# Kernel optimization log

Hardware: AMD Instinct MI355X
Metric: run time of the kernel (lower is better)

## Reference

```python
import jax, jax.numpy as jnp
import numpy as np

B, S, D, H = 2, 2048, 1024, 16
HD = D // H  # head_dim = 64


def setup_inputs() -> dict:
    key = jax.random.key(0)
    ks = jax.random.split(key, 12)
    w_scale = 1.0 / np.sqrt(D)
    return {
        "x": jax.random.normal(ks[0], (B, S, D), dtype=jnp.float32),
        "cause_mask": jax.random.randint(ks[1], (B, S), 0, 2) > 0,
        "effect_mask": jax.random.randint(ks[2], (B, S), 0, 2) > 0,
        "intervention_strength": jnp.float32(1.0),
        "Wq": jax.random.normal(ks[3], (D, D), dtype=jnp.float32) * w_scale,
        "bq": jnp.zeros((D,), dtype=jnp.float32),
        "Wk": jax.random.normal(ks[4], (D, D), dtype=jnp.float32) * w_scale,
        "bk": jnp.zeros((D,), dtype=jnp.float32),
        "Wv": jax.random.normal(ks[5], (D, D), dtype=jnp.float32) * w_scale,
        "bv": jnp.zeros((D,), dtype=jnp.float32),
        "Wo": jax.random.normal(ks[6], (D, D), dtype=jnp.float32) * w_scale,
        "bo": jnp.zeros((D,), dtype=jnp.float32),
    }


def reference(x, cause_mask, effect_mask, intervention_strength,
              Wq, bq, Wk, bk, Wv, bv, Wo, bo):
    b, s, d = x.shape
    # QKV projections -> [b, H, s, HD]
    q = (x @ Wq + bq).reshape(b, s, H, HD).transpose(0, 2, 1, 3)
    k = (x @ Wk + bk).reshape(b, s, H, HD).transpose(0, 2, 1, 3)
    v = (x @ Wv + bv).reshape(b, s, H, HD).transpose(0, 2, 1, 3)

    scores = jnp.einsum("bhqd,bhkd->bhqk", q, k) / jnp.sqrt(jnp.float32(HD))

    # Intervention mask: cause tokens on the query axis, effect on the key axis.
    # Faithful to source: both 'effect_to_cause' and 'cause_to_effect' are the
    # same boolean product, so multiplier = 1 - s*m + 0.5*s*m.
    cm = cause_mask[:, None, :, None]  # [b,1,s,1] query axis
    em = effect_mask[:, None, None, :]  # [b,1,1,s] key axis
    m = (cm & em).astype(scores.dtype)  # [b,1,s,s], broadcasts over heads
    imask = 1.0 - intervention_strength * m + 0.5 * intervention_strength * m
    scores = scores * imask

    attn = jax.nn.softmax(scores, axis=-1)  # dropout is identity in eval
    out = jnp.einsum("bhqk,bhkd->bhqd", attn, v)
    out = out.transpose(0, 2, 1, 3).reshape(b, s, d)
    return out @ Wo + bo
```

## Files before the change

kernel.cpp:

```cpp
#include <hip/hip_runtime.h>
#include <hip/hip_bf16.h>


typedef __attribute__((ext_vector_type(8))) short bf16x8;
typedef __attribute__((ext_vector_type(4))) float f32x4;

__device__ __forceinline__ unsigned short f2b(float f) {
  union { float f; unsigned u; } x; x.f = f;
  unsigned r = x.u + 0x7FFFu + ((x.u >> 16) & 1u);
  return (unsigned short)(r >> 16);
}

__device__ __forceinline__ unsigned short f2b_n(float f) {
  __hip_bfloat16 h = __float2bfloat16(f);
  union { __hip_bfloat16 h; unsigned short u; } c; c.h = h;
  return c.u;
}

__device__ __forceinline__ float fexp2(float x) {
#if __has_builtin(__builtin_amdgcn_exp2f)
  return __builtin_amdgcn_exp2f(x);
#else
  return __expf(x * 0.6931471805599453f);
#endif
}

__device__ __forceinline__ void gl_lds16(const unsigned short* g, unsigned short* l) {
  __builtin_amdgcn_global_load_lds(
      (const __attribute__((address_space(1))) unsigned int*)g,
      (__attribute__((address_space(3))) unsigned int*)l, 16, 0, 0);
}


__global__ __launch_bounds__(256) void cvt_x_kernel(const float* __restrict__ x,
                                                    unsigned short* __restrict__ xb, int n4) {
  int i = blockIdx.x * 256 + threadIdx.x;
  if (i >= n4) return;
  float4 v = ((const float4*)x)[i];
  ushort4 o;
  o.x = f2b(v.x); o.y = f2b(v.y); o.z = f2b(v.z); o.w = f2b(v.w);
  ((ushort4*)xb)[i] = o;
}

__global__ __launch_bounds__(256) void cvt_w4_kernel(
    const float* __restrict__ W0, const float* __restrict__ W1,
    const float* __restrict__ W2, const float* __restrict__ W3,
    unsigned short* __restrict__ WtBase) {
  __shared__ float t[64][33];
  const int z = blockIdx.z;
  const float* W = z == 0 ? W0 : (z == 1 ? W1 : (z == 2 ? W2 : W3));
  unsigned short* Wt = WtBase + (size_t)z * 1048576;
  const int k0 = blockIdx.x * 64, n0 = blockIdx.y * 32;
  const int tx = threadIdx.x, ty = threadIdx.y;
  #pragma unroll
  for (int i = 0; i < 8; i++)
    t[ty + i * 8][tx] = W[(size_t)(k0 + ty + i * 8) * 1024 + n0 + tx];
  __syncthreads();
  #pragma unroll
  for (int i = 0; i < 4; i++) {
    const int n = ty + i * 8;
    ushort2 pk;
    pk.x = f2b(t[tx * 2][n]);
    pk.y = f2b(t[tx * 2 + 1][n]);
    *(ushort2*)&Wt[(size_t)(n0 + n) * 1024 + k0 + tx * 2] = pk;
  }
}

__global__ __launch_bounds__(256) void gemm_qkv(
    const unsigned short* __restrict__ A, const unsigned short* __restrict__ Bt,
    const float* __restrict__ b0, const float* __restrict__ b1, const float* __restrict__ b2,
    unsigned short* __restrict__ dq, unsigned short* __restrict__ dk,
    unsigned short* __restrict__ dv) {
  __shared__ unsigned short As[2][4096];
  __shared__ unsigned short Bs[2][4096];
  const int tid = threadIdx.x;
  const int w = tid >> 6, lane = tid & 63;
  const int li = lane & 15, g = lane >> 4;
  const int wm = w >> 1, wn = w & 1;
  const int m0 = blockIdx.x * 128, n0 = blockIdx.y * 128;

  const int seg0 = w * 2, seg1 = w * 2 + 1;
  const int srow0 = seg0 * 16 + (lane >> 2), srow1 = seg1 * 16 + (lane >> 2);
  const int scol = (lane & 3) * 8;
  const unsigned short* gA0 = A + (size_t)(m0 + srow0) * 1024 + scol;
  const unsigned short* gA1 = A + (size_t)(m0 + srow1) * 1024 + scol;
  const unsigned short* gB0 = Bt + (size_t)(n0 + srow0) * 1024 + scol;
  const unsigned short* gB1 = Bt + (size_t)(n0 + srow1) * 1024 + scol;

  f32x4 acc[4][4];
  #pragma unroll
  for (int i = 0; i < 4; i++)
    #pragma unroll
    for (int j = 0; j < 4; j++) acc[i][j] = (f32x4){0.f, 0.f, 0.f, 0.f};

#define GSTAGE(bufi, kt)                                 \
  {                                                      \
    const int ko = (kt) * 32;                            \
    gl_lds16(gA0 + ko, &As[bufi][seg0 * 512]);           \
    gl_lds16(gA1 + ko, &As[bufi][seg1 * 512]);           \
    gl_lds16(gB0 + ko, &Bs[bufi][seg0 * 512]);           \
    gl_lds16(gB1 + ko, &Bs[bufi][seg1 * 512]);           \
  }

  GSTAGE(0, 0)
  int buf = 0;
  for (int kt = 0; kt < 32; kt++) {
    __syncthreads();
    if (kt + 1 < 32) GSTAGE(buf ^ 1, kt + 1)
    bf16x8 af[4], bfr[4];
    #pragma unroll
    for (int mt = 0; mt < 4; mt++)
      af[mt] = *(const bf16x8*)&As[buf][(wm * 64 + mt * 16 + li) * 32 + g * 8];
    #pragma unroll
    for (int nt = 0; nt < 4; nt++)
      bfr[nt] = *(const bf16x8*)&Bs[buf][(wn * 64 + nt * 16 + li) * 32 + g * 8];
    #pragma unroll
    for (int mt = 0; mt < 4; mt++)
      #pragma unroll
      for (int nt = 0; nt < 4; nt++)
        acc[mt][nt] = __builtin_amdgcn_mfma_f32_16x16x32_bf16(af[mt], bfr[nt], acc[mt][nt], 0, 0, 0);
    buf ^= 1;
  }
#undef GSTAGE

  const int sel = n0 >> 10;
  const float* bp = sel == 0 ? b0 : (sel == 1 ? b1 : b2);
  unsigned short* dst = sel == 0 ? dq : (sel == 1 ? dk : dv);
  #pragma unroll
  for (int nt = 0; nt < 4; nt++) {
    const int gc = n0 + wn * 64 + nt * 16 + li;
    const int c = gc & 1023, h = c >> 6, d = c & 63;
    const float bv = bp[c];
    #pragma unroll
    for (int mt = 0; mt < 4; mt++) {
      const int base = m0 + wm * 64 + mt * 16 + g * 4;
      const int bb = base >> 11, s = base & 2047;
      if (sel < 2) {
        #pragma unroll
        for (int r = 0; r < 4; r++)
          dst[((size_t)(bb * 16 + h) * 2048 + s + r) * 64 + d] = f2b_n(acc[mt][nt][r] + bv);
      } else {
        ushort4 pk;
        pk.x = f2b_n(acc[mt][nt][0] + bv);
        pk.y = f2b_n(acc[mt][nt][1] + bv);
        pk.z = f2b_n(acc[mt][nt][2] + bv);
        pk.w = f2b_n(acc[mt][nt][3] + bv);
        *(ushort4*)&dst[((size_t)(bb * 16 + h) * 64 + d) * 2048 + s] = pk;
      }
    }
  }
}

__global__ __launch_bounds__(256) void gemm_out(
    const unsigned short* __restrict__ A, const unsigned short* __restrict__ Bt,
    const float* __restrict__ bias, float* __restrict__ dout) {
  __shared__ unsigned short As[2][4096];
  __shared__ unsigned short Bs[2][2048];
  const int tid = threadIdx.x;
  const int w = tid >> 6, lane = tid & 63;
  const int li = lane & 15, g = lane >> 4;
  const int m0 = blockIdx.x * 128, n0 = blockIdx.y * 64;

  const int srow0 = w * 32 + (lane >> 2), srow1 = w * 32 + 16 + (lane >> 2);
  const int srowB = w * 16 + (lane >> 2);
  const int scol = (lane & 3) * 8;
  const unsigned short* gA0 = A + (size_t)(m0 + srow0) * 1024 + scol;
  const unsigned short* gA1 = A + (size_t)(m0 + srow1) * 1024 + scol;
  const unsigned short* gB0 = Bt + (size_t)(n0 + srowB) * 1024 + scol;

  f32x4 acc[2][4];
  #pragma unroll
  for (int i = 0; i < 2; i++)
    #pragma unroll
    for (int j = 0; j < 4; j++) acc[i][j] = (f32x4){0.f, 0.f, 0.f, 0.f};

#define OSTAGE(bufi, kt)                                 \
  {                                                      \
    const int ko = (kt) * 32;                            \
    gl_lds16(gA0 + ko, &As[bufi][w * 1024]);             \
    gl_lds16(gA1 + ko, &As[bufi][w * 1024 + 512]);       \
    gl_lds16(gB0 + ko, &Bs[bufi][w * 512]);              \
  }

  OSTAGE(0, 0)
  int buf = 0;
  for (int kt = 0; kt < 32; kt++) {
    __syncthreads();
    if (kt + 1 < 32) OSTAGE(buf ^ 1, kt + 1)
    bf16x8 af[2], bfr[4];
    #pragma unroll
    for (int mt = 0; mt < 2; mt++)
      af[mt] = *(const bf16x8*)&As[buf][(w * 32 + mt * 16 + li) * 32 + g * 8];
    #pragma unroll
    for (int nt = 0; nt < 4; nt++)
      bfr[nt] = *(const bf16x8*)&Bs[buf][(nt * 16 + li) * 32 + g * 8];
    #pragma unroll
    for (int mt = 0; mt < 2; mt++)
      #pragma unroll
      for (int nt = 0; nt < 4; nt++)
        acc[mt][nt] = __builtin_amdgcn_mfma_f32_16x16x32_bf16(af[mt], bfr[nt], acc[mt][nt], 0, 0, 0);
    buf ^= 1;
  }
#undef OSTAGE

  #pragma unroll
  for (int nt = 0; nt < 4; nt++) {
    const int gc = n0 + nt * 16 + li;
    const float bv = bias[gc];
    #pragma unroll
    for (int mt = 0; mt < 2; mt++)
      #pragma unroll
      for (int r = 0; r < 4; r++) {
        const int gr = m0 + w * 32 + mt * 16 + g * 4 + r;
        dout[(size_t)gr * 1024 + gc] = acc[mt][nt][r] + bv;
      }
  }
}

__global__ __launch_bounds__(256, 2) void attn_kernel(
    const unsigned short* __restrict__ qb, const unsigned short* __restrict__ kb,
    const unsigned short* __restrict__ vtb, const int* __restrict__ cause,
    const int* __restrict__ effect, const float* __restrict__ strength,
    unsigned short* __restrict__ attb) {
  __shared__ unsigned short Ks[2][4096];
  __shared__ unsigned short Vs[2][4096];
  __shared__ unsigned short Pl[4][2048];
  const int tid = threadIdx.x;
  const int w = tid >> 6, lane = tid & 63;
  const int g = lane >> 4, li = lane & 15;
  const int lid = blockIdx.y * 16 + blockIdx.x;
  const int bh = ((lid & 7) << 2) | ((lid >> 3) & 3);
  const int qblk = lid >> 5;
  const int b = bh >> 4, h = bh & 15;
  const int q0 = qblk * 128 + w * 32;

  const unsigned short* kbp = kb + (size_t)bh * 2048 * 64;
  const unsigned short* vbp = vtb + (size_t)bh * 64 * 2048;

  bf16x8 qa[2][2];
  #pragma unroll
  for (int i = 0; i < 2; i++) {
    const unsigned short* qrow = qb + ((size_t)bh * 2048 + q0 + i * 16 + li) * 64 + g * 8;
    qa[i][0] = *(const bf16x8*)(qrow);
    qa[i][1] = *(const bf16x8*)(qrow + 32);
  }

  const float LOG2E = 1.44269504f;
  const float fmask = 1.0f - 0.5f * strength[0];
  const float c0s2 = 0.125f * LOG2E;
  const float c1s2 = c0s2 * fmask;
  float mrr[2][4];
  #pragma unroll
  for (int i = 0; i < 2; i++)
    #pragma unroll
    for (int r = 0; r < 4; r++)
      mrr[i][r] = cause[b * 2048 + q0 + i * 16 + g * 4 + r] ? c1s2 : c0s2;
  const int* eff = effect + b * 2048;

  const int seg0 = w * 2, seg1 = w * 2 + 1;
  const int r0 = seg0 * 8 + (lane >> 3), r1 = seg1 * 8 + (lane >> 3);
  const int cs = (((lane & 7) ^ (lane >> 3)) * 8);
  const unsigned short* kg0 = kbp + (size_t)r0 * 64 + cs;
  const unsigned short* kg1 = kbp + (size_t)r1 * 64 + cs;
  const unsigned short* vg0 = vbp + (size_t)r0 * 2048 + cs;
  const unsigned short* vg1 = vbp + (size_t)r1 * 2048 + cs;

#define ASTAGE(bufi, t)                                        \
  {                                                            \
    gl_lds16(kg0 + (size_t)(t) * 4096, &Ks[bufi][seg0 * 512]); \
    gl_lds16(kg1 + (size_t)(t) * 4096, &Ks[bufi][seg1 * 512]); \
    gl_lds16(vg0 + (t) * 64, &Vs[bufi][seg0 * 512]);           \
    gl_lds16(vg1 + (t) * 64, &Vs[bufi][seg1 * 512]);           \
  }

  const int swz = (li & 7) << 4;
  const int col0 = ((g * 16) ^ swz) >> 1;
  const int col1 = ((64 + g * 16) ^ swz) >> 1;

  float l[2][4];
  f32x4 acc[2][4];
  #pragma unroll
  for (int i = 0; i < 2; i++) {
    #pragma unroll
    for (int r = 0; r < 4; r++) l[i][r] = 0.f;
    #pragma unroll
    for (int c = 0; c < 4; c++) acc[i][c] = (f32x4){0.f, 0.f, 0.f, 0.f};
  }

  ASTAGE(0, 0)
  int buf = 0;
  for (int t = 0; t < 32; t++) {
    __syncthreads();
    if (t + 1 < 32) ASTAGE(buf ^ 1, t + 1)
    const int kk = t * 64;
    #pragma unroll
    for (int s = 0; s < 4; s++) {
      const bf16x8 kf0 = *(const bf16x8*)&Ks[buf][s * 1024 + li * 64 + col0];
      const bf16x8 kf1 = *(const bf16x8*)&Ks[buf][s * 1024 + li * 64 + col1];
      const bool eb = eff[kk + s * 16 + li] != 0;
      #pragma unroll
      for (int i = 0; i < 2; i++) {
        f32x4 z = (f32x4){0.f, 0.f, 0.f, 0.f};
        z = __builtin_amdgcn_mfma_f32_16x16x32_bf16(qa[i][0], kf0, z, 0, 0, 0);
        z = __builtin_amdgcn_mfma_f32_16x16x32_bf16(qa[i][1], kf1, z, 0, 0, 0);
        #pragma unroll
        for (int r = 0; r < 4; r++) {
          const float p = fexp2(z[r] * (eb ? mrr[i][r] : c0s2));
          l[i][r] += p;
          const int row = i * 16 + g * 4 + r;
          Pl[w][row * 64 + (((s * 32 + li * 2) ^ ((row & 7) << 4)) >> 1)] = f2b_n(p);
        }
      }
    }
    bf16x8 pa[2][2];
    #pragma unroll
    for (int i = 0; i < 2; i++) {
      pa[i][0] = *(const bf16x8*)&Pl[w][(i * 16 + li) * 64 + col0];
      pa[i][1] = *(const bf16x8*)&Pl[w][(i * 16 + li) * 64 + col1];
    }
    #pragma unroll
    for (int c = 0; c < 4; c++) {
      const bf16x8 vf0 = *(const bf16x8*)&Vs[buf][c * 1024 + li * 64 + col0];
      const bf16x8 vf1 = *(const bf16x8*)&Vs[buf][c * 1024 + li * 64 + col1];
      #pragma unroll
      for (int i = 0; i < 2; i++) {
        acc[i][c] = __builtin_amdgcn_mfma_f32_16x16x32_bf16(pa[i][0], vf0, acc[i][c], 0, 0, 0);
        acc[i][c] = __builtin_amdgcn_mfma_f32_16x16x32_bf16(pa[i][1], vf1, acc[i][c], 0, 0, 0);
      }
    }
    buf ^= 1;
  }
#undef ASTAGE

  #pragma unroll
  for (int off = 1; off < 16; off <<= 1)
    #pragma unroll
    for (int i = 0; i < 2; i++)
      #pragma unroll
      for (int r = 0; r < 4; r++) l[i][r] += __shfl_xor(l[i][r], off, 16);
  #pragma unroll
  for (int i = 0; i < 2; i++)
    #pragma unroll
    for (int r = 0; r < 4; r++) l[i][r] = 1.0f / l[i][r];
  #pragma unroll
  for (int i = 0; i < 2; i++)
    #pragma unroll
    for (int c = 0; c < 4; c++)
      #pragma unroll
      for (int r = 0; r < 4; r++) {
        const int row = q0 + i * 16 + g * 4 + r;
        attb[(size_t)(b * 2048 + row) * 1024 + h * 64 + c * 16 + li] = f2b_n(acc[i][c][r] * l[i][r]);
      }
}


extern "C" void kernel_launch(void* const* d_in, const int* in_sizes, int n_in,
                              void* d_out, int out_size, void* d_ws, size_t ws_size,
                              hipStream_t stream) {
  (void)in_sizes; (void)n_in; (void)out_size; (void)ws_size;
  const float* x = (const float*)d_in[0];
  const int* cause = (const int*)d_in[1];
  const int* effect = (const int*)d_in[2];
  const float* strength = (const float*)d_in[3];
  const float* Wq = (const float*)d_in[4];
  const float* bq = (const float*)d_in[5];
  const float* Wk = (const float*)d_in[6];
  const float* bk = (const float*)d_in[7];
  const float* Wv = (const float*)d_in[8];
  const float* bv = (const float*)d_in[9];
  const float* Wo = (const float*)d_in[10];
  const float* bo = (const float*)d_in[11];
  float* out = (float*)d_out;

  char* ws = (char*)d_ws;
  unsigned short* xb  = (unsigned short*)(ws);
  unsigned short* wqt = (unsigned short*)(ws + (8u << 20));
  unsigned short* qbf = (unsigned short*)(ws + (16u << 20));
  unsigned short* kbf = (unsigned short*)(ws + (24u << 20));
  unsigned short* vtb = (unsigned short*)(ws + (32u << 20));
  unsigned short* wot = wqt + 3u * 1048576u;
  unsigned short* attb = xb;

  cvt_x_kernel<<<4096, 256, 0, stream>>>(x, xb, 1048576);
  cvt_w4_kernel<<<dim3(16, 32, 4), dim3(32, 8), 0, stream>>>(Wq, Wk, Wv, Wo, wqt);

  gemm_qkv<<<dim3(32, 24), 256, 0, stream>>>(xb, wqt, bq, bk, bv, qbf, kbf, vtb);
  attn_kernel<<<dim3(16, 32), 256, 0, stream>>>(qbf, kbf, vtb, cause, effect, strength, attb);
  gemm_out<<<dim3(32, 16), 256, 0, stream>>>(attb, wot, bo, out);
}
```

Measured before the change: 219.6 us.

## Shrink QKV GEMM and attention tiles to launch more blocks per CU

The QKV GEMM tile shrinks from 128x128 to 128x64, doubling the grid and adding a 4-blocks-per-CU launch bound. The attention kernel goes from 256 to 128 threads per block (64 query rows instead of 128), doubling its grid. Attention also drops K/V double buffering for a single buffer with load-then-sync, cutting LDS use so more blocks fit per CU. The aim is better occupancy and wave fill on the many-CU device, at the cost of less operand reuse per block and no longer overlapping K/V loads with compute inside a block.

Result: slower. 231.1 us (+5.2%).

```diff
diff --git a/kernel.cpp b/kernel.cpp
--- a/kernel.cpp
+++ b/kernel.cpp
@@ -66,74 +66,71 @@
   }
 }
 
-__global__ __launch_bounds__(256) void gemm_qkv(
+__global__ __launch_bounds__(256, 4) void gemm_qkv(
     const unsigned short* __restrict__ A, const unsigned short* __restrict__ Bt,
     const float* __restrict__ b0, const float* __restrict__ b1, const float* __restrict__ b2,
     unsigned short* __restrict__ dq, unsigned short* __restrict__ dk,
     unsigned short* __restrict__ dv) {
   __shared__ unsigned short As[2][4096];
-  __shared__ unsigned short Bs[2][4096];
+  __shared__ unsigned short Bs[2][2048];
   const int tid = threadIdx.x;
   const int w = tid >> 6, lane = tid & 63;
   const int li = lane & 15, g = lane >> 4;
-  const int wm = w >> 1, wn = w & 1;
-  const int m0 = blockIdx.x * 128, n0 = blockIdx.y * 128;
-
-  const int seg0 = w * 2, seg1 = w * 2 + 1;
-  const int srow0 = seg0 * 16 + (lane >> 2), srow1 = seg1 * 16 + (lane >> 2);
+  const int m0 = blockIdx.x * 128, n0 = blockIdx.y * 64;
+
+  const int srow0 = w * 32 + (lane >> 2), srow1 = srow0 + 16;
+  const int srowB = w * 16 + (lane >> 2);
   const int scol = (lane & 3) * 8;
   const unsigned short* gA0 = A + (size_t)(m0 + srow0) * 1024 + scol;
   const unsigned short* gA1 = A + (size_t)(m0 + srow1) * 1024 + scol;
-  const unsigned short* gB0 = Bt + (size_t)(n0 + srow0) * 1024 + scol;
-  const unsigned short* gB1 = Bt + (size_t)(n0 + srow1) * 1024 + scol;
-
-  f32x4 acc[4][4];
-  #pragma unroll
-  for (int i = 0; i < 4; i++)
+  const unsigned short* gB0 = Bt + (size_t)(n0 + srowB) * 1024 + scol;
+
+  f32x4 acc[2][4];
+  #pragma unroll
+  for (int i = 0; i < 2; i++)
     #pragma unroll
     for (int j = 0; j < 4; j++) acc[i][j] = (f32x4){0.f, 0.f, 0.f, 0.f};
 
-#define GSTAGE(bufi, kt)                                 \
+#define QSTAGE(bufi, kt)                                 \
   {                                                      \
     const int ko = (kt) * 32;                            \
-    gl_lds16(gA0 + ko, &As[bufi][seg0 * 512]);           \
-    gl_lds16(gA1 + ko, &As[bufi][seg1 * 512]);           \
-    gl_lds16(gB0 + ko, &Bs[bufi][seg0 * 512]);           \
-    gl_lds16(gB1 + ko, &Bs[bufi][seg1 * 512]);           \
-  }
-
-  GSTAGE(0, 0)
+    gl_lds16(gA0 + ko, &As[bufi][w * 1024]);             \
+    gl_lds16(gA1 + ko, &As[bufi][w * 1024 + 512]);       \
+    gl_lds16(gB0 + ko, &Bs[bufi][w * 512]);              \
+  }
+
+  QSTAGE(0, 0)
   int buf = 0;
   for (int kt = 0; kt < 32; kt++) {
     __syncthreads();
-    if (kt + 1 < 32) GSTAGE(buf ^ 1, kt + 1)
-    bf16x8 af[4], bfr[4];
-    #pragma unroll
-    for (int mt = 0; mt < 4; mt++)
-      af[mt] = *(const bf16x8*)&As[buf][(wm * 64 + mt * 16 + li) * 32 + g * 8];
+    if (kt + 1 < 32) QSTAGE(buf ^ 1, kt + 1)
+    bf16x8 af[2], bfr[4];
+    #pragma unroll
+    for (int mt = 0; mt < 2; mt++)
+      af[mt] = *(const bf16x8*)&As[buf][(w * 32 + mt * 16 + li) * 32 + g * 8];
     #pragma unroll
     for (int nt = 0; nt < 4; nt++)
-      bfr[nt] = *(const bf16x8*)&Bs[buf][(wn * 64 + nt * 16 + li) * 32 + g * 8];
-    #pragma unroll
-    for (int mt = 0; mt < 4; mt++)
+      bfr[nt] = *(const bf16x8*)&Bs[buf][(nt * 16 + li) * 32 + g * 8];
+    #pragma unroll
+    for (int mt = 0; mt < 2; mt++)
       #pragma unroll
       for (int nt = 0; nt < 4; nt++)
         acc[mt][nt] = __builtin_amdgcn_mfma_f32_16x16x32_bf16(af[mt], bfr[nt], acc[mt][nt], 0, 0, 0);
     buf ^= 1;
   }
-#undef GSTAGE
+#undef QSTAGE
 
   const int sel = n0 >> 10;
   const float* bp = sel == 0 ? b0 : (sel == 1 ? b1 : b2);
   unsigned short* dst = sel == 0 ? dq : (sel == 1 ? dk : dv);
   #pragma unroll
   for (int nt = 0; nt < 4; nt++) {
-    const int gc = n0 + wn * 64 + nt * 16 + li;
+    const int gc = n0 + nt * 16 + li;
     const int c = gc & 1023, h = c >> 6, d = c & 63;
     const float bv = bp[c];
     #pragma unroll
-    for (int mt = 0; mt < 4; mt++) {
-      const int base = m0 + wm * 64 + mt * 16 + g * 4;
+    for (int mt = 0; mt < 2; mt++) {
+      const int base = m0 + w * 32 + mt * 16 + g * 4;
       const int bb = base >> 11, s = base & 2047;
       if (sel < 2) {
         #pragma unroll
@@ -161,7 +158,7 @@
   const int li = lane & 15, g = lane >> 4;
   const int m0 = blockIdx.x * 128, n0 = blockIdx.y * 64;
 
-  const int srow0 = w * 32 + (lane >> 2), srow1 = w * 32 + 16 + (lane >> 2);
+  const int srow0 = w * 32 + (lane >> 2), srow1 = srow0 + 16;
   const int srowB = w * 16 + (lane >> 2);
   const int scol = (lane & 3) * 8;
   const unsigned short* gA0 = A + (size_t)(m0 + srow0) * 1024 + scol;
@@ -217,22 +214,22 @@
   }
 }
 
-__global__ __launch_bounds__(256, 2) void attn_kernel(
+__global__ __launch_bounds__(128, 3) void attn_kernel(
     const unsigned short* __restrict__ qb, const unsigned short* __restrict__ kb,
     const unsigned short* __restrict__ vtb, const int* __restrict__ cause,
     const int* __restrict__ effect, const float* __restrict__ strength,
     unsigned short* __restrict__ attb) {
-  __shared__ unsigned short Ks[2][4096];
-  __shared__ unsigned short Vs[2][4096];
-  __shared__ unsigned short Pl[4][2048];
+  __shared__ unsigned short Ks[4096];
+  __shared__ unsigned short Vs[4096];
+  __shared__ unsigned short Pl[2][2048];
   const int tid = threadIdx.x;
   const int w = tid >> 6, lane = tid & 63;
   const int g = lane >> 4, li = lane & 15;
-  const int lid = blockIdx.y * 16 + blockIdx.x;
+  const int lid = blockIdx.y * 32 + blockIdx.x;
   const int bh = ((lid & 7) << 2) | ((lid >> 3) & 3);
   const int qblk = lid >> 5;
   const int b = bh >> 4, h = bh & 15;
-  const int q0 = qblk * 128 + w * 32;
+  const int q0 = qblk * 64 + w * 32;
 
   const unsigned short* kbp = kb + (size_t)bh * 2048 * 64;
   const unsigned short* vbp = vtb + (size_t)bh * 64 * 2048;
@@ -257,20 +254,25 @@
       mrr[i][r] = cause[b * 2048 + q0 + i * 16 + g * 4 + r] ? c1s2 : c0s2;
   const int* eff = effect + b * 2048;
 
-  const int seg0 = w * 2, seg1 = w * 2 + 1;
-  const int r0 = seg0 * 8 + (lane >> 3), r1 = seg1 * 8 + (lane >> 3);
-  const int cs = (((lane & 7) ^ (lane >> 3)) * 8);
-  const unsigned short* kg0 = kbp + (size_t)r0 * 64 + cs;
-  const unsigned short* kg1 = kbp + (size_t)r1 * 64 + cs;
-  const unsigned short* vg0 = vbp + (size_t)r0 * 2048 + cs;
-  const unsigned short* vg1 = vbp + (size_t)r1 * 2048 + cs;
-
-#define ASTAGE(bufi, t)                                        \
-  {                                                            \
-    gl_lds16(kg0 + (size_t)(t) * 4096, &Ks[bufi][seg0 * 512]); \
-    gl_lds16(kg1 + (size_t)(t) * 4096, &Ks[bufi][seg1 * 512]); \
-    gl_lds16(vg0 + (t) * 64, &Vs[bufi][seg0 * 512]);           \
-    gl_lds16(vg1 + (t) * 64, &Vs[bufi][seg1 * 512]);           \
+  const int rowin = lane >> 3;
+  const int cs = (((lane & 7) ^ rowin) * 8);
+  const unsigned short* kg[4];
+  const unsigned short* vg[4];
+  #pragma unroll
+  for (int j = 0; j < 4; j++) {
+    const int seg = w * 4 + j;
+    const int row = seg * 8 + rowin;
+    kg[j] = kbp + (size_t)row * 64 + cs;
+    vg[j] = vbp + (size_t)row * 2048 + cs;
+  }
+
+#define ASTAGE(t)                                            \
+  {                                                          \
+    _Pragma("unroll")                                        \
+    for (int j = 0; j < 4; j++) {                            \
+      gl_lds16(kg[j] + (size_t)(t) * 4096, &Ks[(w * 4 + j) * 512]); \
+      gl_lds16(vg[j] + (t) * 64, &Vs[(w * 4 + j) * 512]);    \
+    }                                                        \
   }
 
   const int swz = (li & 7) << 4;
@@ -287,16 +289,15 @@
     for (int c = 0; c < 4; c++) acc[i][c] = (f32x4){0.f, 0.f, 0.f, 0.f};
   }
 
-  ASTAGE(0, 0)
-  int buf = 0;
   for (int t = 0; t < 32; t++) {
+    if (t) __syncthreads();
+    ASTAGE(t)
     __syncthreads();
-    if (t + 1 < 32) ASTAGE(buf ^ 1, t + 1)
     const int kk = t * 64;
     #pragma unroll
     for (int s = 0; s < 4; s++) {
-      const bf16x8 kf0 = *(const bf16x8*)&Ks[buf][s * 1024 + li * 64 + col0];
-      const bf16x8 kf1 = *(const bf16x8*)&Ks[buf][s * 1024 + li * 64 + col1];
+      const bf16x8 kf0 = *(const bf16x8*)&Ks[s * 1024 + li * 64 + col0];
+      const bf16x8 kf1 = *(const bf16x8*)&Ks[s * 1024 + li * 64 + col1];
       const bool eb = eff[kk + s * 16 + li] != 0;
       #pragma unroll
       for (int i = 0; i < 2; i++) {
@@ -320,15 +321,14 @@
     }
     #pragma unroll
     for (int c = 0; c < 4; c++) {
-      const bf16x8 vf0 = *(const bf16x8*)&Vs[buf][c * 1024 + li * 64 + col0];
-      const bf16x8 vf1 = *(const bf16x8*)&Vs[buf][c * 1024 + li * 64 + col1];
+      const bf16x8 vf0 = *(const bf16x8*)&Vs[c * 1024 + li * 64 + col0];
+      const bf16x8 vf1 = *(const bf16x8*)&Vs[c * 1024 + li * 64 + col1];
       #pragma unroll
       for (int i = 0; i < 2; i++) {
         acc[i][c] = __builtin_amdgcn_mfma_f32_16x16x32_bf16(pa[i][0], vf0, acc[i][c], 0, 0, 0);
         acc[i][c] = __builtin_amdgcn_mfma_f32_16x16x32_bf16(pa[i][1], vf1, acc[i][c], 0, 0, 0);
       }
     }
-    buf ^= 1;
   }
 #undef ASTAGE
 
@@ -384,7 +384,7 @@
   cvt_x_kernel<<<4096, 256, 0, stream>>>(x, xb, 1048576);
   cvt_w4_kernel<<<dim3(16, 32, 4), dim3(32, 8), 0, stream>>>(Wq, Wk, Wv, Wo, wqt);
 
-  gemm_qkv<<<dim3(32, 24), 256, 0, stream>>>(xb, wqt, bq, bk, bv, qbf, kbf, vtb);
-  attn_kernel<<<dim3(16, 32), 256, 0, stream>>>(qbf, kbf, vtb, cause, effect, strength, attb);
+  gemm_qkv<<<dim3(32, 48), 256, 0, stream>>>(xb, wqt, bq, bk, bv, qbf, kbf, vtb);
+  attn_kernel<<<dim3(32, 32), 128, 0, stream>>>(qbf, kbf, vtb, cause, effect, strength, attb);
   gemm_out<<<dim3(32, 16), 256, 0, stream>>>(attb, wot, bo, out);
 }
```
